# Kernel tuning notes

Measured on AMD Instinct MI355X. Metric: run time of the kernel, lower is better.

Reference implementation:

```python
import jax, jax.numpy as jnp
import numpy as np

N_NODES = 50000


def gcn_conv(x, edge_index, W, b):
    """PyG GCNConv: add self-loops, sym-normalize, out = A_hat @ (x W) + b."""
    src, dst = edge_index[0], edge_index[1]
    n = x.shape[0]
    h = x @ W  # [N, out]
    # degree with self-loops (all edge weights = 1)
    deg = jax.ops.segment_sum(jnp.ones_like(dst, dtype=x.dtype), dst, num_segments=n) + 1.0
    dinv = jax.lax.rsqrt(deg)  # deg >= 1 so safe
    norm = dinv[src] * dinv[dst]  # [E]
    msgs = h[src] * norm[:, None]  # gather + scale
    agg = jax.ops.segment_sum(msgs, dst, num_segments=n)  # scatter-add
    agg = agg + h * (dinv * dinv)[:, None]  # self-loop term: norm_ii = dinv_i^2
    return agg + b


def setup_inputs() -> dict:
    key = jax.random.key(0)
    k_x, k_e, k_w1, k_w2 = jax.random.split(key, 4)
    in_ch, hid, out_ch = 256, 128, 128
    x = jax.random.normal(k_x, (N_NODES, in_ch), dtype=jnp.float32)
    edge_index = jax.random.randint(k_e, (2, 1_600_000), 0, N_NODES, dtype=jnp.int32)
    # Glorot-style init like PyG GCNConv
    W1 = jax.random.normal(k_w1, (in_ch, hid), dtype=jnp.float32) * (1.0 / np.sqrt(in_ch))
    b1 = jnp.zeros((hid,), dtype=jnp.float32)
    W2 = jax.random.normal(k_w2, (hid, out_ch), dtype=jnp.float32) * (1.0 / np.sqrt(hid))
    b2 = jnp.zeros((out_ch,), dtype=jnp.float32)
    return {"x": x, "edge_index": edge_index, "W1": W1, "b1": b1, "W2": W2, "b2": b2}


def reference(x, edge_index, W1, b1, W2, b2):
    # layer 1: GCNConv -> ReLU (dropout is identity in eval mode)
    h = jax.nn.relu(gcn_conv(x, edge_index, W1, b1))
    # layer 2: GCNConv -> ReLU
    out = jax.nn.relu(gcn_conv(h, edge_index, W2, b2))
    return out
```

## Files before the change

### kernel.cpp

```cpp
#include <hip/hip_runtime.h>
#include <cstdint>
#include <cstddef>


#define ELL_STRIDE 64
#define BUCK_SZ 64
#define BCAP 4096
#define OVF_CAP 1024
#define PART_T 2048
#define CUR_STRIDE 32

typedef __attribute__((ext_vector_type(8))) short bf16x8;
typedef __attribute__((ext_vector_type(4))) float floatx4;

__device__ __forceinline__ unsigned short f2bf(float f) {
  unsigned int u = __float_as_uint(f);
  unsigned int r = (u + 0x7fffu + ((u >> 16) & 1u)) >> 16;
  return (unsigned short)r;
}
__device__ __forceinline__ float2 bfpair(unsigned int p) {
  float2 r;
  r.x = __uint_as_float(p << 16);
  r.y = __uint_as_float(p & 0xffff0000u);
  return r;
}

__global__ __launch_bounds__(256) void k_cvt_w(const float* __restrict__ W1,
                                               const float* __restrict__ W2,
                                               unsigned short* __restrict__ WT1,
                                               unsigned short* __restrict__ WT2,
                                               int* __restrict__ cursor,
                                               int* __restrict__ ovf_cnt,
                                               unsigned short* __restrict__ hb,
                                               int N, int NB) {
  int i = blockIdx.x * 256 + threadIdx.x;
  if (i < NB) cursor[(size_t)i * CUR_STRIDE] = 0;
  if (i == NB) *ovf_cnt = 0;
  if (i < 128) {
    int chunk = i >> 5, j = i & 31;
    hb[(size_t)chunk * (N + 1) * 32 + (size_t)N * 32 + j] = 0;
  }
  if (i < 128 * 256) {
    int n = i >> 8, k = i & 255;
    WT1[i] = f2bf(W1[k * 128 + n]);
  } else if (i < 128 * 256 + 128 * 128) {
    int j = i - 128 * 256;
    int n = j >> 7, k = j & 127;
    WT2[j] = f2bf(W2[k * 128 + n]);
  }
}

__global__ __launch_bounds__(256) void k_part(const int* __restrict__ src,
                                              const int* __restrict__ dst,
                                              int* __restrict__ cursor,
                                              unsigned int* __restrict__ part,
                                              int* __restrict__ ovf_cnt,
                                              int* __restrict__ ovf,
                                              int E, int NB) {
  __shared__ unsigned int stage1[PART_T];
  __shared__ unsigned int stage2[PART_T];
  __shared__ int hist[1024];
  __shared__ int base_g[1024];
  __shared__ int base_l[1024];
  __shared__ int cl[1024];
  __shared__ int sc[256];
  const int tid = threadIdx.x;
  const int e0 = blockIdx.x * PART_T;
  int valid = E - e0; if (valid > PART_T) valid = PART_T;

  #pragma unroll
  for (int j = 0; j < 4; ++j) { hist[tid + j * 256] = 0; cl[tid + j * 256] = 0; }
  __syncthreads();
  for (int i = tid; i < valid; i += 256) {
    int e = e0 + i;
    unsigned int v = (unsigned int)(src[e] & 0xffff) | ((unsigned int)dst[e] << 16);
    stage1[i] = v;
    atomicAdd(&hist[(v >> 16) >> 6], 1);
  }
  __syncthreads();
  for (int b = tid; b < NB; b += 256) {
    int h = hist[b];
    if (h) base_g[b] = atomicAdd(&cursor[(size_t)b * CUR_STRIDE], h);
  }
  int h0 = hist[4 * tid], h1 = hist[4 * tid + 1];
  int h2 = hist[4 * tid + 2], h3 = hist[4 * tid + 3];
  int pv = h0 + h1 + h2 + h3;
  sc[tid] = pv;
  __syncthreads();
  #pragma unroll
  for (int off = 1; off < 256; off <<= 1) {
    int t = (tid >= off) ? sc[tid - off] : 0;
    __syncthreads();
    sc[tid] += t;
    __syncthreads();
  }
  int excl = sc[tid] - pv;
  base_l[4 * tid] = excl;
  base_l[4 * tid + 1] = excl + h0;
  base_l[4 * tid + 2] = excl + h0 + h1;
  base_l[4 * tid + 3] = excl + h0 + h1 + h2;
  __syncthreads();
  for (int i = tid; i < valid; i += 256) {
    unsigned int v = stage1[i];
    int b = (v >> 16) >> 6;
    int pos = base_l[b] + atomicAdd(&cl[b], 1);
    stage2[pos] = v;
  }
  __syncthreads();
  for (int i = tid; i < valid; i += 256) {
    unsigned int v = stage2[i];
    int b = (v >> 16) >> 6;
    int g = base_g[b] + (i - base_l[b]);
    if (g < BCAP) {
      part[(size_t)b * BCAP + g] = v;
    } else {
      int p = atomicAdd(ovf_cnt, 1);
      if (p < OVF_CAP) { ovf[2 * p] = (int)(v & 0xffffu); ovf[2 * p + 1] = (int)(v >> 16); }
    }
  }
}

__global__ __launch_bounds__(256) void k_fill2(const unsigned int* __restrict__ part,
                                               const int* __restrict__ cursor,
                                               unsigned short* __restrict__ col,
                                               int* __restrict__ cnt,
                                               float* __restrict__ dinv,
                                               int* __restrict__ ovf_cnt,
                                               int* __restrict__ ovf, int N) {
  __shared__ unsigned short slab[BUCK_SZ * ELL_STRIDE];
  __shared__ int cl[BUCK_SZ];
  const int tid = threadIdx.x;
  const int b = blockIdx.x;
  if (tid < BUCK_SZ) cl[tid] = 0;
  {
    unsigned int dpk = ((unsigned int)N << 16) | (unsigned int)N;
    unsigned int* s32 = (unsigned int*)slab;
    #pragma unroll
    for (int i = 0; i < (BUCK_SZ * ELL_STRIDE / 2) / 256; ++i)
      s32[i * 256 + tid] = dpk;
  }
  __syncthreads();
  int count = cursor[(size_t)b * CUR_STRIDE]; if (count > BCAP) count = BCAP;
  const unsigned int* p = part + (size_t)b * BCAP;
  for (int i = tid; i < count; i += 256) {
    unsigned int v = p[i];
    int row = (v >> 16) & (BUCK_SZ - 1);
    int k = atomicAdd(&cl[row], 1);
    if (k < ELL_STRIDE) {
      slab[row * ELL_STRIDE + k] = (unsigned short)(v & 0xffffu);
    } else {
      int q = atomicAdd(ovf_cnt, 1);
      if (q < OVF_CAP) { ovf[2 * q] = (int)(v & 0xffffu); ovf[2 * q + 1] = (int)(v >> 16); }
    }
  }
  __syncthreads();
  uint4* d4 = (uint4*)(col + (size_t)b * BUCK_SZ * ELL_STRIDE);
  const uint4* s4 = (const uint4*)slab;
  #pragma unroll
  for (int i = 0; i < (BUCK_SZ * ELL_STRIDE * 2) / (16 * 256); ++i)
    d4[i * 256 + tid] = s4[i * 256 + tid];
  if (tid < BUCK_SZ) {
    int node = b * BUCK_SZ + tid;
    if (node < N) {
      int c = cl[tid];
      cnt[node] = c;
      dinv[node] = rsqrtf((float)c + 1.0f);
    }
  }
}

template <int K, bool AF32>
__global__ __launch_bounds__(512) void k_gemm_mfma(const void* __restrict__ Xv,
                                                   const unsigned short* __restrict__ WT,
                                                   const float* __restrict__ dinv,
                                                   unsigned short* __restrict__ hb,
                                                   int M) {
  constexpr int KP = K + 8;
  __shared__ unsigned short Bs[128 * KP];
  const int tid = threadIdx.x;
  const int wave = tid >> 6, lane = tid & 63;
  const int q = lane >> 4, m = lane & 15;
  const int row0 = blockIdx.x * 128 + wave * 16;
  const bool active = row0 < M;
  const int arow = row0 + m;

  for (int c = tid; c < 128 * (K / 8); c += 512) {
    int r = c / (K / 8), ko = (c % (K / 8)) * 8;
    *(uint4*)(Bs + r * KP + ko) = *(const uint4*)(WT + (size_t)r * K + ko);
  }

  bf16x8 af[K / 32];
  if (active) {
    #pragma unroll
    for (int ks = 0; ks < K / 32; ++ks) {
      const int k0 = ks * 32 + q * 8;
      if (AF32) {
        const float* X = (const float*)Xv;
        float4 a0 = *(const float4*)(X + (size_t)arow * K + k0);
        float4 a1 = *(const float4*)(X + (size_t)arow * K + k0 + 4);
        af[ks] = (bf16x8){(short)f2bf(a0.x), (short)f2bf(a0.y),
                          (short)f2bf(a0.z), (short)f2bf(a0.w),
                          (short)f2bf(a1.x), (short)f2bf(a1.y),
                          (short)f2bf(a1.z), (short)f2bf(a1.w)};
      } else {
        af[ks] = *(const bf16x8*)((const unsigned short*)Xv +
                                  (size_t)arow * K + k0);
      }
    }
  }
  __syncthreads();
  if (!active) return;

  floatx4 acc[8];
  #pragma unroll
  for (int nt = 0; nt < 8; ++nt) acc[nt] = (floatx4){0.f, 0.f, 0.f, 0.f};
  #pragma unroll
  for (int ks = 0; ks < K / 32; ++ks) {
    const int k0 = ks * 32 + q * 8;
    #pragma unroll
    for (int nt = 0; nt < 8; ++nt) {
      bf16x8 bf = *(const bf16x8*)(Bs + (nt * 16 + m) * KP + k0);
      acc[nt] = __builtin_amdgcn_mfma_f32_16x16x32_bf16(af[ks], bf, acc[nt], 0, 0, 0);
    }
  }
  #pragma unroll
  for (int r = 0; r < 4; ++r) {
    int grow = row0 + q * 4 + r;
    float di = dinv[grow];
    #pragma unroll
    for (int nt = 0; nt < 8; ++nt)
      hb[(size_t)(nt >> 1) * (M + 1) * 32 + (size_t)grow * 32 + (nt & 1) * 16 + m] =
          f2bf(acc[nt][r] * di);
  }
}

template <bool BF16OUT>
__global__ __launch_bounds__(256) void k_agg(const uint4* __restrict__ hb4,
                                             const int* __restrict__ cnt,
                                             const unsigned short* __restrict__ col,
                                             const float* __restrict__ dinv,
                                             const int* __restrict__ ovf_cnt,
                                             const int* __restrict__ ovf,
                                             const float* __restrict__ bias,
                                             void* __restrict__ outv, int n) {
  __shared__ unsigned short cols[64][72];
  const int tid = threadIdx.x;
  const int chunk = blockIdx.x & 3;
  const int nd0 = (blockIdx.x >> 2) * 64;
  {
    unsigned int dpk = ((unsigned int)n << 16) | (unsigned int)n;
    int s = tid * 16;
    int node = s >> 6, off = s & 63;
    uint4 v0 = make_uint4(dpk, dpk, dpk, dpk), v1 = v0;
    if (nd0 + node < n) {
      v0 = *(const uint4*)(col + (size_t)(nd0 + node) * ELL_STRIDE + off);
      v1 = *(const uint4*)(col + (size_t)(nd0 + node) * ELL_STRIDE + off + 8);
    }
    *(uint4*)&cols[node][off] = v0;
    *(uint4*)&cols[node][off + 8] = v1;
  }
  __syncthreads();
  const int wave = tid >> 6, lane = tid & 63;
  const int nodeL = wave * 16 + (lane >> 2);
  const int q = lane & 3;
  const int d = nd0 + nodeL;
  const bool valid = d < n;
  const uint4* slab = hb4 + (size_t)chunk * (n + 1) * 4;
  const unsigned short* lc = cols[nodeL];

  float a0 = 0.f, a1 = 0.f, a2 = 0.f, a3 = 0.f;
  float a4 = 0.f, a5 = 0.f, a6 = 0.f, a7 = 0.f;
#define ADDP(P)                                                            \
  {                                                                        \
    float2 x0 = bfpair((P).x), x1 = bfpair((P).y);                         \
    float2 x2 = bfpair((P).z), x3 = bfpair((P).w);                         \
    a0 += x0.x; a1 += x0.y; a2 += x1.x; a3 += x1.y;                        \
    a4 += x2.x; a5 += x2.y; a6 += x3.x; a7 += x3.y;                        \
  }
  if (valid) {
    uint4 p = slab[(size_t)d * 4 + q];
    ADDP(p)
  }
  int m = valid ? cnt[d] : 0; if (m > ELL_STRIDE) m = ELL_STRIDE;
  int mmax = m;
  #pragma unroll
  for (int s = 4; s < 64; s <<= 1) {
    int o = __shfl_xor(mmax, s);
    mmax = o > mmax ? o : mmax;
  }
  for (int k = 0; k < mmax; k += 8) {
    ushort4 ca = *(const ushort4*)(lc + k);
    ushort4 cb = *(const ushort4*)(lc + k + 4);
    uint4 p0 = slab[(size_t)ca.x * 4 + q];
    uint4 p1 = slab[(size_t)ca.y * 4 + q];
    uint4 p2 = slab[(size_t)ca.z * 4 + q];
    uint4 p3 = slab[(size_t)ca.w * 4 + q];
    uint4 p4 = slab[(size_t)cb.x * 4 + q];
    uint4 p5 = slab[(size_t)cb.y * 4 + q];
    uint4 p6 = slab[(size_t)cb.z * 4 + q];
    uint4 p7 = slab[(size_t)cb.w * 4 + q];
    ADDP(p0) ADDP(p1) ADDP(p2) ADDP(p3)
    ADDP(p4) ADDP(p5) ADDP(p6) ADDP(p7)
  }
  if (valid) {
    int V = *ovf_cnt; if (V > OVF_CAP) V = OVF_CAP;
    for (int j = 0; j < V; ++j) {
      if (ovf[2 * j + 1] == d) {
        uint4 p = slab[(size_t)ovf[2 * j] * 4 + q];
        ADDP(p)
      }
    }
  }
#undef ADDP
  if (!valid) return;
  float di = dinv[d];
  float4 b0 = *(const float4*)(bias + chunk * 32 + q * 8);
  float4 b1 = *(const float4*)(bias + chunk * 32 + q * 8 + 4);
  float r0 = fmaxf(di * a0 + b0.x, 0.f);
  float r1 = fmaxf(di * a1 + b0.y, 0.f);
  float r2 = fmaxf(di * a2 + b0.z, 0.f);
  float r3 = fmaxf(di * a3 + b0.w, 0.f);
  float r4 = fmaxf(di * a4 + b1.x, 0.f);
  float r5 = fmaxf(di * a5 + b1.y, 0.f);
  float r6 = fmaxf(di * a6 + b1.z, 0.f);
  float r7 = fmaxf(di * a7 + b1.w, 0.f);
  if (BF16OUT) {
    uint4 pk;
    pk.x = (unsigned int)f2bf(r0) | ((unsigned int)f2bf(r1) << 16);
    pk.y = (unsigned int)f2bf(r2) | ((unsigned int)f2bf(r3) << 16);
    pk.z = (unsigned int)f2bf(r4) | ((unsigned int)f2bf(r5) << 16);
    pk.w = (unsigned int)f2bf(r6) | ((unsigned int)f2bf(r7) << 16);
    ((uint4*)outv)[(size_t)d * 16 + chunk * 4 + q] = pk;
  } else {
    float* o = (float*)outv + (size_t)d * 128 + chunk * 32 + q * 8;
    *(float4*)o = make_float4(r0, r1, r2, r3);
    *(float4*)(o + 4) = make_float4(r4, r5, r6, r7);
  }
}

extern "C" void kernel_launch(void* const* d_in, const int* in_sizes, int n_in,
                              void* d_out, int out_size, void* d_ws, size_t ws_size,
                              hipStream_t stream) {
  const float* x  = (const float*)d_in[0];
  const int*   ei = (const int*)d_in[1];
  const float* W1 = (const float*)d_in[2];
  const float* b1 = (const float*)d_in[3];
  const float* W2 = (const float*)d_in[4];
  const float* b2 = (const float*)d_in[5];
  float* out = (float*)d_out;

  const int IN_CH = 256;
  const int N = in_sizes[0] / IN_CH;
  const int E = in_sizes[1] / 2;
  const int NB = (N + BUCK_SZ - 1) / BUCK_SZ;

  const int* src = ei;
  const int* dst = ei + E;

  char* ws = (char*)d_ws;
  size_t off = 0;
  auto carve = [&](size_t bytes) {
    void* p = ws + off;
    off += (bytes + 255) & ~(size_t)255;
    return p;
  };
  int*            cursor  = (int*)carve((size_t)NB * CUR_STRIDE * 4);
  int*            ovf_cnt = (int*)carve(256);
  int*            ovf     = (int*)carve((size_t)OVF_CAP * 2 * 4);
  int*            cnt     = (int*)carve((size_t)N * 4);
  float*          dinv    = (float*)carve((size_t)N * 4);
  unsigned short* col     = (unsigned short*)carve((size_t)NB * BUCK_SZ * ELL_STRIDE * 2);
  unsigned short* hb      = (unsigned short*)carve((size_t)(N + 1) * 256);
  unsigned short* WT1     = (unsigned short*)carve(128 * 256 * 2);
  unsigned short* WT2     = (unsigned short*)carve(128 * 128 * 2);
  char*           unionp  = (char*)carve((size_t)NB * BCAP * 4);
  unsigned int*   part    = (unsigned int*)unionp;
  unsigned short* aggbuf  = (unsigned short*)unionp;

  k_cvt_w<<<(128 * 256 + 128 * 128 + 255) / 256, 256, 0, stream>>>(
      W1, W2, WT1, WT2, cursor, ovf_cnt, hb, N, NB);
  k_part <<<(E + PART_T - 1) / PART_T, 256, 0, stream>>>(src, dst, cursor, part,
                                                         ovf_cnt, ovf, E, NB);
  k_fill2<<<NB, 256, 0, stream>>>(part, cursor, col, cnt, dinv, ovf_cnt, ovf, N);

  int gblocks = (N + 127) / 128;
  int ablocks = 4 * ((N + 63) / 64);
  k_gemm_mfma<256, true ><<<gblocks, 512, 0, stream>>>(x, WT1, dinv, hb, N);
  k_agg<true ><<<ablocks, 256, 0, stream>>>((const uint4*)hb, cnt, col, dinv,
                                            ovf_cnt, ovf, b1, aggbuf, N);
  k_gemm_mfma<128, false><<<gblocks, 512, 0, stream>>>(aggbuf, WT2, dinv, hb, N);
  k_agg<false><<<ablocks, 256, 0, stream>>>((const uint4*)hb, cnt, col, dinv,
                                            ovf_cnt, ovf, b2, out, N);
}
```

Measured before the change: 245.6 us.

## Partition edges into coarse 1024-node buckets and filter per fine bucket in fill

The edge partition pass now bins edges by destination into roughly 49 coarse buckets of 1024 nodes instead of about 782 buckets of 64. It also processes 4096 edges per block. This cuts global cursor atomics and gives longer contiguous write runs in the partition kernel. In exchange, each fill block has to scan its whole coarse bucket and keep only the 1/16 of entries that match its fine bucket, which multiplies the reads of the partition buffer by about sixteen.

```diff
diff --git a/kernel.cpp b/kernel.cpp
--- a/kernel.cpp
+++ b/kernel.cpp
@@ -5,9 +5,10 @@
 
 #define ELL_STRIDE 64
 #define BUCK_SZ 64
-#define BCAP 4096
+#define COARSE_SH 10
+#define BCAP1 36864
 #define OVF_CAP 1024
-#define PART_T 2048
+#define PART_T 4096
 #define CUR_STRIDE 32
 
 typedef __attribute__((ext_vector_type(8))) short bf16x8;
@@ -32,10 +33,10 @@
                                                int* __restrict__ cursor,
                                                int* __restrict__ ovf_cnt,
                                                unsigned short* __restrict__ hb,
-                                               int N, int NB) {
+                                               int N, int NBC) {
   int i = blockIdx.x * 256 + threadIdx.x;
-  if (i < NB) cursor[(size_t)i * CUR_STRIDE] = 0;
-  if (i == NB) *ovf_cnt = 0;
+  if (i < NBC) cursor[(size_t)i * CUR_STRIDE] = 0;
+  if (i == NBC) *ovf_cnt = 0;
   if (i < 128) {
     int chunk = i >> 5, j = i & 31;
     hb[(size_t)chunk * (N + 1) * 32 + (size_t)N * 32 + j] = 0;
@@ -56,36 +57,30 @@
                                               unsigned int* __restrict__ part,
                                               int* __restrict__ ovf_cnt,
                                               int* __restrict__ ovf,
-                                              int E, int NB) {
+                                              int E) {
   __shared__ unsigned int stage1[PART_T];
   __shared__ unsigned int stage2[PART_T];
-  __shared__ int hist[1024];
-  __shared__ int base_g[1024];
-  __shared__ int base_l[1024];
-  __shared__ int cl[1024];
+  __shared__ int hist[256];
+  __shared__ int base_g[256];
+  __shared__ int base_l[256];
+  __shared__ int cl[256];
   __shared__ int sc[256];
   const int tid = threadIdx.x;
   const int e0 = blockIdx.x * PART_T;
   int valid = E - e0; if (valid > PART_T) valid = PART_T;
 
-  #pragma unroll
-  for (int j = 0; j < 4; ++j) { hist[tid + j * 256] = 0; cl[tid + j * 256] = 0; }
+  hist[tid] = 0; cl[tid] = 0;
   __syncthreads();
   for (int i = tid; i < valid; i += 256) {
     int e = e0 + i;
     unsigned int v = (unsigned int)(src[e] & 0xffff) | ((unsigned int)dst[e] << 16);
     stage1[i] = v;
-    atomicAdd(&hist[(v >> 16) >> 6], 1);
-  }
-  __syncthreads();
-  for (int b = tid; b < NB; b += 256) {
-    int h = hist[b];
-    if (h) base_g[b] = atomicAdd(&cursor[(size_t)b * CUR_STRIDE], h);
-  }
-  int h0 = hist[4 * tid], h1 = hist[4 * tid + 1];
-  int h2 = hist[4 * tid + 2], h3 = hist[4 * tid + 3];
-  int pv = h0 + h1 + h2 + h3;
-  sc[tid] = pv;
+    atomicAdd(&hist[v >> (16 + COARSE_SH)], 1);
+  }
+  __syncthreads();
+  int h = hist[tid];
+  if (h) base_g[tid] = atomicAdd(&cursor[(size_t)tid * CUR_STRIDE], h);
+  sc[tid] = h;
   __syncthreads();
   #pragma unroll
   for (int off = 1; off < 256; off <<= 1) {
@@ -94,25 +89,21 @@
     sc[tid] += t;
     __syncthreads();
   }
-  int excl = sc[tid] - pv;
-  base_l[4 * tid] = excl;
-  base_l[4 * tid + 1] = excl + h0;
-  base_l[4 * tid + 2] = excl + h0 + h1;
-  base_l[4 * tid + 3] = excl + h0 + h1 + h2;
+  base_l[tid] = sc[tid] - h;
   __syncthreads();
   for (int i = tid; i < valid; i += 256) {
     unsigned int v = stage1[i];
-    int b = (v >> 16) >> 6;
+    int b = v >> (16 + COARSE_SH);
     int pos = base_l[b] + atomicAdd(&cl[b], 1);
     stage2[pos] = v;
   }
   __syncthreads();
   for (int i = tid; i < valid; i += 256) {
     unsigned int v = stage2[i];
-    int b = (v >> 16) >> 6;
+    int b = v >> (16 + COARSE_SH);
     int g = base_g[b] + (i - base_l[b]);
-    if (g < BCAP) {
-      part[(size_t)b * BCAP + g] = v;
+    if (g < BCAP1) {
+      part[(size_t)b * BCAP1 + g] = v;
     } else {
       int p = atomicAdd(ovf_cnt, 1);
       if (p < OVF_CAP) { ovf[2 * p] = (int)(v & 0xffffu); ovf[2 * p + 1] = (int)(v >> 16); }
@@ -131,6 +122,7 @@
   __shared__ int cl[BUCK_SZ];
   const int tid = threadIdx.x;
   const int b = blockIdx.x;
+  const int c = b >> 4;
   if (tid < BUCK_SZ) cl[tid] = 0;
   {
     unsigned int dpk = ((unsigned int)N << 16) | (unsigned int)N;
@@ -140,17 +132,19 @@
       s32[i * 256 + tid] = dpk;
   }
   __syncthreads();
-  int count = cursor[(size_t)b * CUR_STRIDE]; if (count > BCAP) count = BCAP;
-  const unsigned int* p = part + (size_t)b * BCAP;
+  int count = cursor[(size_t)c * CUR_STRIDE]; if (count > BCAP1) count = BCAP1;
+  const unsigned int* p = part + (size_t)c * BCAP1;
   for (int i = tid; i < count; i += 256) {
     unsigned int v = p[i];
-    int row = (v >> 16) & (BUCK_SZ - 1);
-    int k = atomicAdd(&cl[row], 1);
-    if (k < ELL_STRIDE) {
-      slab[row * ELL_STRIDE + k] = (unsigned short)(v & 0xffffu);
-    } else {
-      int q = atomicAdd(ovf_cnt, 1);
-      if (q < OVF_CAP) { ovf[2 * q] = (int)(v & 0xffffu); ovf[2 * q + 1] = (int)(v >> 16); }
+    if ((v >> 22) == (unsigned int)b) {
+      int row = (v >> 16) & (BUCK_SZ - 1);
+      int k = atomicAdd(&cl[row], 1);
+      if (k < ELL_STRIDE) {
+        slab[row * ELL_STRIDE + k] = (unsigned short)(v & 0xffffu);
+      } else {
+        int q = atomicAdd(ovf_cnt, 1);
+        if (q < OVF_CAP) { ovf[2 * q] = (int)(v & 0xffffu); ovf[2 * q + 1] = (int)(v >> 16); }
+      }
     }
   }
   __syncthreads();
@@ -162,9 +156,9 @@
   if (tid < BUCK_SZ) {
     int node = b * BUCK_SZ + tid;
     if (node < N) {
-      int c = cl[tid];
-      cnt[node] = c;
-      dinv[node] = rsqrtf((float)c + 1.0f);
+      int c2 = cl[tid];
+      cnt[node] = c2;
+      dinv[node] = rsqrtf((float)c2 + 1.0f);
     }
   }
 }
@@ -352,7 +346,8 @@
   const int IN_CH = 256;
   const int N = in_sizes[0] / IN_CH;
   const int E = in_sizes[1] / 2;
-  const int NB = (N + BUCK_SZ - 1) / BUCK_SZ;
+  const int NBF = (N + BUCK_SZ - 1) / BUCK_SZ;
+  const int NBC = (N + (1 << COARSE_SH) - 1) >> COARSE_SH;
 
   const int* src = ei;
   const int* dst = ei + E;
@@ -364,24 +359,24 @@
     off += (bytes + 255) & ~(size_t)255;
     return p;
   };
-  int*            cursor  = (int*)carve((size_t)NB * CUR_STRIDE * 4);
+  int*            cursor  = (int*)carve((size_t)NBC * CUR_STRIDE * 4);
   int*            ovf_cnt = (int*)carve(256);
   int*            ovf     = (int*)carve((size_t)OVF_CAP * 2 * 4);
   int*            cnt     = (int*)carve((size_t)N * 4);
   float*          dinv    = (float*)carve((size_t)N * 4);
-  unsigned short* col     = (unsigned short*)carve((size_t)NB * BUCK_SZ * ELL_STRIDE * 2);
+  unsigned short* col     = (unsigned short*)carve((size_t)NBF * BUCK_SZ * ELL_STRIDE * 2);
   unsigned short* hb      = (unsigned short*)carve((size_t)(N + 1) * 256);
   unsigned short* WT1     = (unsigned short*)carve(128 * 256 * 2);
   unsigned short* WT2     = (unsigned short*)carve(128 * 128 * 2);
-  char*           unionp  = (char*)carve((size_t)NB * BCAP * 4);
+  char*           unionp  = (char*)carve((size_t)N * 128 * 2);
   unsigned int*   part    = (unsigned int*)unionp;
   unsigned short* aggbuf  = (unsigned short*)unionp;
 
   k_cvt_w<<<(128 * 256 + 128 * 128 + 255) / 256, 256, 0, stream>>>(
-      W1, W2, WT1, WT2, cursor, ovf_cnt, hb, N, NB);
+      W1, W2, WT1, WT2, cursor, ovf_cnt, hb, N, NBC);
   k_part <<<(E + PART_T - 1) / PART_T, 256, 0, stream>>>(src, dst, cursor, part,
-                                                         ovf_cnt, ovf, E, NB);
-  k_fill2<<<NB, 256, 0, stream>>>(part, cursor, col, cnt, dinv, ovf_cnt, ovf, N);
+                                                         ovf_cnt, ovf, E);
+  k_fill2<<<NBF, 256, 0, stream>>>(part, cursor, col, cnt, dinv, ovf_cnt, ovf, N);
 
   int gblocks = (N + 127) / 128;
   int ablocks = 4 * ((N + 63) / 64);
```

Result: slower. 267.8 us (+9.0%).
